# Performance work log

Measured on AMD Instinct MI355X. Metric: run time of the kernel, lower is better.

The kernel has to match this reference:

```python
import jax, jax.numpy as jnp
import numpy as np
from jax import lax

# ---- static config (matches init_kwargs) ----
STRIDE = 16
BASE_SIZE = 16
SCALES = np.array([2., 4., 8., 16., 32.])
RATIOS = np.array([0.5, 1., 2.])
CLIP = 4.14
NMS_THRESH = 0.7
PRE_NMS = 6000
POST_NMS = 300
MIN_SIZE = 16.0


def _whctrs(a):
    w = a[2] - a[0] + 1.0
    h = a[3] - a[1] + 1.0
    return w, h, a[0] + 0.5 * (w - 1.0), a[1] + 0.5 * (h - 1.0)


def _mkanchors(ws, hs, xc, yc):
    return np.stack([xc - 0.5 * (ws - 1.0), yc - 0.5 * (hs - 1.0),
                     xc + 0.5 * (ws - 1.0), yc + 0.5 * (hs - 1.0)], axis=1)


def _base_anchors():
    ba = np.array([1.0, 1.0, BASE_SIZE, BASE_SIZE]) - 1.0
    w, h, xc, yc = _whctrs(ba)
    size = w * h
    ws = np.round(np.sqrt(size / RATIOS))
    hs = np.round(ws * RATIOS)
    ra = _mkanchors(ws, hs, xc, yc)
    out = []
    for i in range(ra.shape[0]):
        w, h, xc, yc = _whctrs(ra[i])
        out.append(_mkanchors(w * SCALES, h * SCALES, xc, yc))
    return np.concatenate(out, axis=0)  # (A,4), A = len(ratios)*len(scales)


def _grid_anchors(Hf, Wf):
    ba = _base_anchors()                       # (A,4)
    sx, sy = np.meshgrid(np.arange(Wf) * STRIDE, np.arange(Hf) * STRIDE)
    shifts = np.stack([sx, sy, sx, sy], axis=-1)          # (Hf,Wf,4)
    anch = shifts[:, :, None, :] + ba[None, None, :, :]    # (Hf,Wf,A,4)
    return jnp.asarray(anch.reshape(1, -1, 4), dtype=jnp.float32)


def _decode_clip(anchors, deltas, img_h, img_w):
    # NormalizedBoxCenterDecoder (stds=1) + clip to image
    aw = anchors[..., 2] - anchors[..., 0]
    ah = anchors[..., 3] - anchors[..., 1]
    ax = anchors[..., 0] + 0.5 * aw
    ay = anchors[..., 1] + 0.5 * ah
    dx, dy, dw, dh = deltas[..., 0], deltas[..., 1], deltas[..., 2], deltas[..., 3]
    ox = dx * aw + ax
    oy = dy * ah + ay
    ow = jnp.exp(jnp.minimum(dw, CLIP)) * aw * 0.5
    oh = jnp.exp(jnp.minimum(dh, CLIP)) * ah * 0.5
    x1 = jnp.clip(ox - ow, 0.0, img_w - 1.0)
    y1 = jnp.clip(oy - oh, 0.0, img_h - 1.0)
    x2 = jnp.clip(ox + ow, 0.0, img_w - 1.0)
    y2 = jnp.clip(oy + oh, 0.0, img_h - 1.0)
    return jnp.stack([x1, y1, x2, y2], axis=-1)


def _nms_single(scores, boxes):
    # scores (N,), boxes (N,4). Greedy NMS, force_suppress, sorted by score desc.
    order = jnp.argsort(-scores)[:PRE_NMS]
    s = scores[order]
    b = boxes[order]
    x1, y1, x2, y2 = b[:, 0], b[:, 1], b[:, 2], b[:, 3]
    area = (x2 - x1) * (y2 - y1)
    iw = jnp.maximum(jnp.minimum(x2[:, None], x2[None, :]) - jnp.maximum(x1[:, None], x1[None, :]), 0.0)
    ih = jnp.maximum(jnp.minimum(y2[:, None], y2[None, :]) - jnp.maximum(y1[:, None], y1[None, :]), 0.0)
    inter = iw * ih
    iou = inter / (area[:, None] + area[None, :] - inter + 1e-12)  # (PRE,PRE)

    supp0 = s < 0.0  # invalid entries (score set to -1 by min_size filter)

    def body(supp, i):
        keep = jnp.logical_not(supp[i])
        new = jnp.where(keep, jnp.logical_or(supp, iou[i] > NMS_THRESH), supp)
        new = new.at[i].set(supp[i])  # never self-suppress
        return new, None

    supp, _ = lax.scan(body, supp0, jnp.arange(PRE_NMS))
    kept = jnp.logical_not(supp)
    perm = jnp.argsort(jnp.where(kept, 0, 1), stable=True)  # kept boxes first, order preserved
    out_s = jnp.where(kept[perm], s[perm], -1.0)
    out_b = jnp.where(kept[perm][:, None], b[perm], -1.0)
    return out_s[:POST_NMS, None], out_b[:POST_NMS]


def _forward(img, x, conv_w, conv_b, score_w, score_b, loc_w, loc_b):
    B, _, Hf, Wf = x.shape
    img_h, img_w = float(img.shape[2]), float(img.shape[3])
    anchors = _grid_anchors(Hf, Wf)  # (1, Hf*Wf*A, 4)

    # conv1 3x3 pad 1 + ReLU
    h = lax.conv_general_dilated(x, conv_w, (1, 1), [(1, 1), (1, 1)],
                                 dimension_numbers=('NCHW', 'OIHW', 'NCHW'))
    h = jax.nn.relu(h + conv_b[None, :, None, None])

    A = score_w.shape[0]
    raw_scores = jnp.einsum('bchw,oc->bhwo', h, score_w.reshape(A, -1)) + score_b
    raw_scores = raw_scores.reshape(B, -1, 1)                       # (B,N,1)
    raw_boxes = jnp.einsum('bchw,oc->bhwo', h, loc_w.reshape(4 * A, -1)) + loc_b
    raw_boxes = raw_boxes.reshape(B, -1, 4)                         # (B,N,4)

    rpn_scores = jax.nn.sigmoid(raw_scores)

    roi = _decode_clip(anchors, raw_boxes, img_h, img_w)            # (B,N,4)
    width = roi[..., 2] - roi[..., 0]
    height = roi[..., 3] - roi[..., 1]
    invalid = jnp.logical_or(width < MIN_SIZE, height < MIN_SIZE)   # (B,N)
    score = jnp.where(invalid[..., None], -1.0, rpn_scores)         # (B,N,1)
    roi = jnp.where(invalid[..., None], -1.0, roi)

    out_s, out_b = jax.vmap(_nms_single)(score[..., 0], roi)        # (B,300,1),(B,300,4)
    return jnp.concatenate([out_s, out_b], axis=-1)                 # (B,300,5)


def setup_inputs() -> dict:
    key = jax.random.key(0)
    ks = jax.random.split(key, 8)
    img = jax.random.normal(ks[0], (1, 3, 1024, 1024), jnp.float32)
    x = jax.random.normal(ks[1], (1, 1024, 64, 64), jnp.float32)
    conv_w = jax.random.normal(ks[2], (1024, 1024, 3, 3), jnp.float32) * 0.01
    conv_b = jnp.zeros((1024,), jnp.float32)
    score_w = jax.random.normal(ks[3], (15, 1024, 1, 1), jnp.float32) * 0.01
    score_b = jnp.zeros((15,), jnp.float32)
    loc_w = jax.random.normal(ks[4], (60, 1024, 1, 1), jnp.float32) * 0.002
    loc_b = jnp.zeros((60,), jnp.float32)
    return {"img": img, "x": x, "conv_w": conv_w, "conv_b": conv_b,
            "score_w": score_w, "score_b": score_b, "loc_w": loc_w, "loc_b": loc_b}


def reference(img, x, conv_w, conv_b, score_w, score_b, loc_w, loc_b):
    return _forward(img, x, conv_w, conv_b, score_w, score_b, loc_w, loc_b)
```

## Files before the change

kernel.cpp:

```cpp
#include <hip/hip_runtime.h>

typedef unsigned int uint;
typedef unsigned short ushort;
typedef unsigned long long u64;

typedef __attribute__((ext_vector_type(8))) short short8;
typedef __attribute__((ext_vector_type(4))) float floatx4;

__device__ inline ushort bf16rne(float v) {
  uint b = __float_as_uint(v);
  uint r = (b + 0x7fffu + ((b >> 16) & 1u)) >> 16;
  return (ushort)r;
}

__device__ inline void gl_lds16(const void* g, void* l) {
  __builtin_amdgcn_global_load_lds(
      (const __attribute__((address_space(1))) unsigned int*)g,
      (__attribute__((address_space(3))) unsigned int*)l, 16, 0, 0);
}

__global__ __launch_bounds__(256) void prep_x(const float* __restrict__ x,
                                              ushort* __restrict__ xh,
                                              ushort* __restrict__ xl) {
  __shared__ float tile[64 * 65];
  int ci0 = blockIdx.x * 64, y = blockIdx.y, t = threadIdx.x;
#pragma unroll
  for (int it = 0; it < 16; ++it) {
    int L = t + 256 * it;
    int cl = L >> 6, xx = L & 63;
    tile[cl * 65 + xx] = x[(size_t)(ci0 + cl) * 4096 + y * 64 + xx];
  }
  __syncthreads();
#pragma unroll
  for (int it = 0; it < 16; ++it) {
    int L = t + 256 * it;
    int xx = L >> 6, cl = L & 63;
    float v = tile[cl * 65 + xx];
    ushort h2 = bf16rne(v);
    float hf = __uint_as_float((uint)h2 << 16);
    ushort l2 = bf16rne(v - hf);
    size_t oi = ((size_t)((y + 1) * 66 + (xx + 1))) * 1024 + ci0 + cl;
    xh[oi] = h2;
    xl[oi] = l2;
  }
}

__global__ __launch_bounds__(256) void prep_w(const float* __restrict__ w,
                                              ushort* __restrict__ wh,
                                              ushort* __restrict__ wl) {
  __shared__ float tile[2304];
  int co = blockIdx.x, ci0 = blockIdx.y * 256, t = threadIdx.x;
  const float* src = w + ((size_t)co * 1024 + ci0) * 9;
  for (int i = t; i < 2304; i += 256) tile[i] = src[i];
  __syncthreads();
  int ci = ci0 + t;
#pragma unroll
  for (int off = 0; off < 9; ++off) {
    float v = tile[t * 9 + off];
    ushort h2 = bf16rne(v);
    float hf = __uint_as_float((uint)h2 << 16);
    ushort l2 = bf16rne(v - hf);
    size_t oi = ((size_t)off << 20) | ((size_t)co << 10) | (size_t)ci;
    wh[oi] = h2;
    wl[oi] = l2;
  }
}

__global__ __launch_bounds__(256) void prep_head(
    const float* __restrict__ score_w, const float* __restrict__ loc_w,
    const float* __restrict__ score_b, const float* __restrict__ loc_b,
    ushort* __restrict__ wh, ushort* __restrict__ wl, float* __restrict__ bh) {
  int idx = blockIdx.x * 256 + threadIdx.x;
  int o = idx >> 10, ci = idx & 1023;
  float v = 0.f;
  if (o < 15) v = score_w[o * 1024 + ci];
  else if (o < 75) v = loc_w[(o - 15) * 1024 + ci];
  ushort h2 = bf16rne(v);
  float hf = __uint_as_float((uint)h2 << 16);
  wh[idx] = h2;
  wl[idx] = bf16rne(v - hf);
  if (idx < 128) bh[idx] = (idx < 15) ? score_b[idx] : ((idx < 75) ? loc_b[idx - 15] : 0.f);
}

template <int IM2COL>
__global__ __launch_bounds__(256, 1) void gemm_bf16x3(
    const ushort* __restrict__ Ahi, const ushort* __restrict__ Alo,
    const ushort* __restrict__ Bhi, const ushort* __restrict__ Blo,
    const float* __restrict__ bias, int nChunks, float* __restrict__ outRaw,
    ushort* __restrict__ outHi, ushort* __restrict__ outLo) {
  __shared__ ushort sm[2 * 4 * 128 * 32];
  const int t = threadIdx.x;
  const int m0 = blockIdx.x * 128;
  const int n0 = blockIdx.y * 128;

  auto stage = [&](int kc, int bufIdx) {
    char* lds = (char*)sm + bufIdx * 32768;
    int off = 0, cc = 0, oy = 0, ox = 0;
    if (IM2COL) {
      off = kc >> 5;
      cc = (kc & 31) << 5;
      oy = off / 3;
      ox = off - 3 * oy;
    }
#pragma unroll
    for (int q = 0; q < 2; ++q) {
      int L = t + 256 * q, row = L >> 2, seg = L & 3;
      size_t aoff, boff;
      if (IM2COL) {
        int m = m0 + row, y = m >> 6, xq = m & 63;
        aoff = ((size_t)((y + oy) * 66 + (xq + ox)) * 1024 + (size_t)cc) * 2 + seg * 16;
        boff = (((size_t)off << 20) + ((size_t)(n0 + row) << 10) + (size_t)cc) * 2 + seg * 16;
      } else {
        aoff = (((size_t)(m0 + row) << 10) + (size_t)kc * 32) * 2 + seg * 16;
        boff = (((size_t)(n0 + row) << 10) + (size_t)kc * 32) * 2 + seg * 16;
      }
      int dst = L * 16;
      gl_lds16((const char*)Ahi + aoff, lds + dst);
      gl_lds16((const char*)Alo + aoff, lds + 8192 + dst);
      gl_lds16((const char*)Bhi + boff, lds + 16384 + dst);
      gl_lds16((const char*)Blo + boff, lds + 24576 + dst);
    }
  };

  const int lane = t & 63, wv = t >> 6;
  const int wm = (wv & 1) * 64, wn = (wv >> 1) * 64;
  const int arow = wm + (lane & 15);
  const int brow = wn + (lane & 15);
  const int ko = (lane >> 4) * 8;

  floatx4 acc[4][4];
#pragma unroll
  for (int i = 0; i < 4; ++i)
#pragma unroll
    for (int j = 0; j < 4; ++j) acc[i][j] = (floatx4){0.f, 0.f, 0.f, 0.f};

  stage(0, 0);
  for (int kc = 0; kc < nChunks; ++kc) {
    __syncthreads();
    if (kc + 1 < nChunks) stage(kc + 1, (kc + 1) & 1);
    const ushort* sb = sm + (kc & 1) * 16384;
    const ushort* sAh = sb;
    const ushort* sAl = sb + 4096;
    const ushort* sBh = sb + 8192;
    const ushort* sBl = sb + 12288;
    short8 ah[4], al[4], bh2[4], bl2[4];
#pragma unroll
    for (int i = 0; i < 4; ++i) {
      ah[i] = *(const short8*)(sAh + (arow + 16 * i) * 32 + ko);
      al[i] = *(const short8*)(sAl + (arow + 16 * i) * 32 + ko);
      bh2[i] = *(const short8*)(sBh + (brow + 16 * i) * 32 + ko);
      bl2[i] = *(const short8*)(sBl + (brow + 16 * i) * 32 + ko);
    }
#pragma unroll
    for (int i = 0; i < 4; ++i)
#pragma unroll
      for (int j = 0; j < 4; ++j) {
        acc[i][j] = __builtin_amdgcn_mfma_f32_16x16x32_bf16(ah[i], bh2[j], acc[i][j], 0, 0, 0);
        acc[i][j] = __builtin_amdgcn_mfma_f32_16x16x32_bf16(ah[i], bl2[j], acc[i][j], 0, 0, 0);
        acc[i][j] = __builtin_amdgcn_mfma_f32_16x16x32_bf16(al[i], bh2[j], acc[i][j], 0, 0, 0);
      }
  }

#pragma unroll
  for (int i = 0; i < 4; ++i)
#pragma unroll
    for (int j = 0; j < 4; ++j) {
      int nn = n0 + wn + 16 * j + (lane & 15);
      float bv = bias[nn];
#pragma unroll
      for (int r = 0; r < 4; ++r) {
        int mm = m0 + wm + 16 * i + (lane >> 4) * 4 + r;
        float v = acc[i][j][r] + bv;
        if (IM2COL) {
          v = fmaxf(v, 0.f);
          ushort h2 = bf16rne(v);
          float hf = __uint_as_float((uint)h2 << 16);
          ushort l2 = bf16rne(v - hf);
          outHi[(size_t)mm * 1024 + nn] = h2;
          outLo[(size_t)mm * 1024 + nn] = l2;
        } else {
          outRaw[(size_t)mm * 128 + nn] = v;
        }
      }
    }
}

__global__ __launch_bounds__(256) void decode_k(const float* __restrict__ raw,
                                                float* __restrict__ scores,
                                                float4* __restrict__ boxes,
                                                uint* __restrict__ key32,
                                                uint* __restrict__ hist) {
  int i = blockIdx.x * 256 + threadIdx.x;
  int m = i / 15, a = i - m * 15;
  int y = m >> 6, x = m & 63;
  const float* rp = raw + (size_t)m * 128;
  float logit = rp[a];
  float dx = rp[15 + 4 * a], dy = rp[16 + 4 * a];
  float dw = rp[17 + 4 * a], dh = rp[18 + 4 * a];
  int rr = a / 5, ss = a - rr * 5;
  float sc5 = (float)(2 << ss);
  float W = ((rr == 0) ? 23.f : (rr == 1) ? 16.f : 11.f) * sc5;
  float H = ((rr == 0) ? 12.f : (rr == 1) ? 16.f : 22.f) * sc5;
  float aw = W - 1.f, ah = H - 1.f;
  float ax = x * 16.f + 7.5f, ay = y * 16.f + 7.5f;
  float ox = dx * aw + ax, oyc = dy * ah + ay;
  float ow = expf(fminf(dw, 4.14f)) * aw * 0.5f;
  float oh = expf(fminf(dh, 4.14f)) * ah * 0.5f;
  float x1 = fminf(fmaxf(ox - ow, 0.f), 1023.f);
  float y1 = fminf(fmaxf(oyc - oh, 0.f), 1023.f);
  float x2 = fminf(fmaxf(ox + ow, 0.f), 1023.f);
  float y2 = fminf(fmaxf(oyc + oh, 0.f), 1023.f);
  bool inval = ((x2 - x1) < 16.f) || ((y2 - y1) < 16.f);
  float sc = inval ? -1.f : (1.f / (1.f + expf(-logit)));
  scores[i] = sc;
  boxes[i] = inval ? make_float4(-1.f, -1.f, -1.f, -1.f) : make_float4(x1, y1, x2, y2);
  uint kb = __float_as_uint(sc);
  uint key = (kb & 0x80000000u) ? ~kb : (kb | 0x80000000u);
  key32[i] = key;
  atomicAdd(&hist[key >> 16], 1u);
}

__global__ __launch_bounds__(256) void find_t16(const uint* __restrict__ hist,
                                                uint* __restrict__ selT) {
  __shared__ uint ps[256];
  __shared__ int segS;
  int t = threadIdx.x;
  uint s = 0;
  const uint* hp = hist + t * 256;
  for (int i = 0; i < 256; ++i) s += hp[i];
  ps[t] = s;
  __syncthreads();
  for (int d = 1; d < 256; d <<= 1) {
    uint v = ps[t] + ((t + d < 256) ? ps[t + d] : 0u);
    __syncthreads();
    ps[t] = v;
    __syncthreads();
  }
  if (ps[t] >= 6000u && (t == 255 || ps[t + 1] < 6000u)) segS = t;
  __syncthreads();
  int sg = segS;
  uint base = (sg == 255) ? 0u : ps[sg + 1];
  uint h2 = hist[sg * 256 + t];
  __syncthreads();
  ps[t] = h2;
  __syncthreads();
  for (int d = 1; d < 256; d <<= 1) {
    uint v = ps[t] + ((t + d < 256) ? ps[t + d] : 0u);
    __syncthreads();
    ps[t] = v;
    __syncthreads();
  }
  if (base + ps[t] >= 6000u && (t == 255 || base + ps[t + 1] < 6000u))
    *selT = (uint)(sg * 256 + t);
}

__global__ __launch_bounds__(256) void gather_k(const uint* __restrict__ key32,
                                                const uint* __restrict__ selT,
                                                uint* __restrict__ cnt,
                                                u64* __restrict__ cand) {
  int i = blockIdx.x * 256 + threadIdx.x;
  uint T = *selT;
  uint k = key32[i];
  if ((k >> 16) >= T) {
    uint pos = atomicAdd(cnt, 1u);
    if (pos < 8192) cand[pos] = ((u64)k << 32) | (u64)(~(uint)i);
  }
}

__global__ __launch_bounds__(1024) void sort_gather(
    const u64* __restrict__ cand, const uint* __restrict__ cnt,
    const float* __restrict__ scores, const float4* __restrict__ boxes,
    float* __restrict__ sortedS, float4* __restrict__ sortedB) {
  extern __shared__ u64 sk[];
  int t = threadIdx.x;
  int C = (int)*cnt;
  if (C > 8192) C = 8192;
  for (int j = t; j < 8192; j += 1024) sk[j] = (j < C) ? cand[j] : 0ull;
  __syncthreads();
  for (int k = 2; k <= 8192; k <<= 1) {
    for (int j2 = k >> 1; j2 > 0; j2 >>= 1) {
      for (int p = t; p < 4096; p += 1024) {
        int i = ((p & ~(j2 - 1)) << 1) | (p & (j2 - 1));
        int ix = i | j2;
        u64 a = sk[i], b = sk[ix];
        bool ddir = (i & k) != 0;
        if ((a < b) != ddir) { sk[i] = b; sk[ix] = a; }
      }
      __syncthreads();
    }
  }
  for (int j = t; j < 6016; j += 1024) {
    if (j < 6000) {
      u64 key = sk[j];
      uint idx = ~(uint)(key & 0xffffffffu);
      sortedS[j] = scores[idx];
      sortedB[j] = boxes[idx];
    } else {
      sortedS[j] = -1.f;
      sortedB[j] = make_float4(0.f, 0.f, 0.f, 0.f);
    }
  }
}

__global__ __launch_bounds__(64) void iou_mask(const float4* __restrict__ boxes,
                                               u64* __restrict__ mask) {
  __shared__ float cx1[64], cy1[64], cx2[64], cy2[64], car[64];
  int bi = blockIdx.x, bj = blockIdx.y, t = threadIdx.x;
  float4 cb = boxes[bj * 64 + t];
  cx1[t] = cb.x; cy1[t] = cb.y; cx2[t] = cb.z; cy2[t] = cb.w;
  car[t] = (cb.z - cb.x) * (cb.w - cb.y);
  __syncthreads();
  int r = bi * 64 + t;
  float4 rb = boxes[r];
  float ra = (rb.z - rb.x) * (rb.w - rb.y);
  u64 wd = 0;
#pragma unroll 8
  for (int j = 0; j < 64; ++j) {
    float iw = fmaxf(fminf(rb.z, cx2[j]) - fmaxf(rb.x, cx1[j]), 0.f);
    float ih = fmaxf(fminf(rb.w, cy2[j]) - fmaxf(rb.y, cy1[j]), 0.f);
    float inter = iw * ih;
    float iou = inter / (ra + car[j] - inter + 1e-12f);
    if (iou > 0.7f && r != bj * 64 + j) wd |= (1ull << j);
  }
  mask[(size_t)r * 128 + bj] = wd;
}

__global__ __launch_bounds__(64) void nms_scan(const u64* __restrict__ mask,
                                               const float* __restrict__ sortedS,
                                               const float4* __restrict__ sortedB,
                                               float* __restrict__ out) {
  __shared__ int klist[300];
  int lane = threadIdx.x;
  u64 Sx = 0, Sy = 0;
  for (int w2 = 0; w2 < 94; ++w2) {
    bool neg = sortedS[w2 * 64 + lane] < 0.f;
    u64 m2 = __ballot(neg);
    if ((w2 >> 1) == lane) { if (w2 & 1) Sy = m2; else Sx = m2; }
  }
  int count = 0;
  for (int w2 = 0; w2 < 94; ++w2) {
    u64 cur = __shfl((w2 & 1) ? Sy : Sx, w2 >> 1);
    u64 rem = ~cur;
    if (w2 == 93) rem &= (1ull << 48) - 1;
    while (rem) {
      int b = __builtin_ctzll(rem);
      int i = w2 * 64 + b;
      if (lane == 0) klist[count] = i;
      count++;
      if (count == 300) goto done;
      const ulonglong2* rp = (const ulonglong2*)(mask + (size_t)i * 128);
      ulonglong2 rv = rp[lane];
      Sx |= rv.x;
      Sy |= rv.y;
      u64 cur2 = __shfl((w2 & 1) ? Sy : Sx, w2 >> 1);
      rem &= ~cur2;
      rem &= (b == 63) ? 0ull : (~0ull << (b + 1));
    }
  }
done:
  __syncthreads();
  for (int j = lane; j < 300; j += 64) {
    float s;
    float4 bb;
    if (j < count) {
      int i = klist[j];
      s = sortedS[i];
      bb = sortedB[i];
    } else {
      s = -1.f;
      bb = make_float4(-1.f, -1.f, -1.f, -1.f);
    }
    out[j * 5 + 0] = s;
    out[j * 5 + 1] = bb.x;
    out[j * 5 + 2] = bb.y;
    out[j * 5 + 3] = bb.z;
    out[j * 5 + 4] = bb.w;
  }
}

constexpr size_t O_XH = 0;
constexpr size_t O_XL = 8921088;
constexpr size_t O_WTH = 17842176;
constexpr size_t O_WTL = 36716544;
constexpr size_t O_HH = 55590912;
constexpr size_t O_HL = 63979520;
constexpr size_t O_WHH = 72368128;
constexpr size_t O_WHL = 72630272;
constexpr size_t O_BHD = 72892416;
constexpr size_t O_SC = 72892928;
constexpr size_t O_BX = 73138688;
constexpr size_t O_KEY = 74121728;
constexpr size_t O_HIST = 74367488;
constexpr size_t O_CNT = 74629632;
constexpr size_t O_CAND = 74629888;
constexpr size_t O_SELT = 74695424;
constexpr size_t O_SS = 74695680;
constexpr size_t O_SB = 74719744;
constexpr size_t O_RAW = 0;
constexpr size_t O_MASK = 17842176;

extern "C" void kernel_launch(void* const* d_in, const int* in_sizes, int n_in,
                              void* d_out, int out_size, void* d_ws,
                              size_t ws_size, hipStream_t stream) {
  (void)in_sizes; (void)n_in; (void)out_size; (void)ws_size;
  const float* x = (const float*)d_in[1];
  const float* conv_w = (const float*)d_in[2];
  const float* conv_b = (const float*)d_in[3];
  const float* score_w = (const float*)d_in[4];
  const float* score_b = (const float*)d_in[5];
  const float* loc_w = (const float*)d_in[6];
  const float* loc_b = (const float*)d_in[7];
  float* out = (float*)d_out;
  char* ws = (char*)d_ws;

  ushort* xh = (ushort*)(ws + O_XH);
  ushort* xl = (ushort*)(ws + O_XL);
  ushort* wTh = (ushort*)(ws + O_WTH);
  ushort* wTl = (ushort*)(ws + O_WTL);
  ushort* hh = (ushort*)(ws + O_HH);
  ushort* hl = (ushort*)(ws + O_HL);
  ushort* wHh = (ushort*)(ws + O_WHH);
  ushort* wHl = (ushort*)(ws + O_WHL);
  float* biasH = (float*)(ws + O_BHD);
  float* raw = (float*)(ws + O_RAW);
  float* scores = (float*)(ws + O_SC);
  float4* boxes = (float4*)(ws + O_BX);
  uint* key32 = (uint*)(ws + O_KEY);
  uint* hist = (uint*)(ws + O_HIST);
  uint* cnt = (uint*)(ws + O_CNT);
  u64* cand = (u64*)(ws + O_CAND);
  uint* selT = (uint*)(ws + O_SELT);
  float* sortedS = (float*)(ws + O_SS);
  float4* sortedB = (float4*)(ws + O_SB);
  u64* mask = (u64*)(ws + O_MASK);

  hipMemsetAsync(ws + O_XH, 0, 2 * 8921088, stream);
  hipMemsetAsync(ws + O_HIST, 0, 262144 + 256, stream);

  prep_x<<<dim3(16, 64), 256, 0, stream>>>(x, xh, xl);
  prep_w<<<dim3(1024, 4), 256, 0, stream>>>(conv_w, wTh, wTl);
  prep_head<<<512, 256, 0, stream>>>(score_w, loc_w, score_b, loc_b, wHh, wHl, biasH);

  gemm_bf16x3<1><<<dim3(32, 8), 256, 0, stream>>>(xh, xl, wTh, wTl, conv_b, 288,
                                                  nullptr, hh, hl);
  gemm_bf16x3<0><<<dim3(32, 1), 256, 0, stream>>>(hh, hl, wHh, wHl, biasH, 32,
                                                  raw, nullptr, nullptr);

  decode_k<<<240, 256, 0, stream>>>(raw, scores, boxes, key32, hist);
  find_t16<<<1, 256, 0, stream>>>(hist, selT);
  gather_k<<<240, 256, 0, stream>>>(key32, selT, cnt, cand);
  sort_gather<<<1, 1024, 65536, stream>>>(cand, cnt, scores, boxes, sortedS, sortedB);
  iou_mask<<<dim3(94, 94), 64, 0, stream>>>(sortedB, mask);
  nms_scan<<<1, 64, 0, stream>>>(mask, sortedS, sortedB, out);
}
```

Before: 743.9 us.

## Swizzle GEMM LDS layout, replace bitonic sort with bucket rank, prune NMS work

The GEMM staging now writes LDS in MFMA-fragment order, so each lane reads a contiguous 16-byte slice and LDS bank conflicts drop. The single-block 8192-element bitonic sort is replaced by a 4096-bucket histogram scatter followed by an in-bucket rank, which cuts the many barrier-separated passes. The IoU mask kernel skips lower-triangle tiles that the scan never reads. The NMS scan prefetches the next candidate's mask row and stops early once 300 boxes are kept. The bucket rank costs quadratic work if many candidates share a bucket, and it uses an extra workspace buffer.

```diff
diff --git a/kernel.cpp b/kernel.cpp
--- a/kernel.cpp
+++ b/kernel.cpp
@@ -104,15 +104,17 @@
     }
 #pragma unroll
     for (int q = 0; q < 2; ++q) {
-      int L = t + 256 * q, row = L >> 2, seg = L & 3;
+      int L = t + 256 * q;
+      int g = L >> 6, ko = (L >> 4) & 3, row = L & 15;
+      int gr = g * 16 + row;
       size_t aoff, boff;
       if (IM2COL) {
-        int m = m0 + row, y = m >> 6, xq = m & 63;
-        aoff = ((size_t)((y + oy) * 66 + (xq + ox)) * 1024 + (size_t)cc) * 2 + seg * 16;
-        boff = (((size_t)off << 20) + ((size_t)(n0 + row) << 10) + (size_t)cc) * 2 + seg * 16;
+        int m = m0 + gr, y = m >> 6, xq = m & 63;
+        aoff = ((size_t)((y + oy) * 66 + (xq + ox)) * 1024 + (size_t)cc + ko * 8) * 2;
+        boff = (((size_t)off << 20) + ((size_t)(n0 + gr) << 10) + (size_t)cc + ko * 8) * 2;
       } else {
-        aoff = (((size_t)(m0 + row) << 10) + (size_t)kc * 32) * 2 + seg * 16;
-        boff = (((size_t)(n0 + row) << 10) + (size_t)kc * 32) * 2 + seg * 16;
+        aoff = (((size_t)(m0 + gr) << 10) + (size_t)kc * 32 + ko * 8) * 2;
+        boff = (((size_t)(n0 + gr) << 10) + (size_t)kc * 32 + ko * 8) * 2;
       }
       int dst = L * 16;
       gl_lds16((const char*)Ahi + aoff, lds + dst);
@@ -124,9 +126,6 @@
 
   const int lane = t & 63, wv = t >> 6;
   const int wm = (wv & 1) * 64, wn = (wv >> 1) * 64;
-  const int arow = wm + (lane & 15);
-  const int brow = wn + (lane & 15);
-  const int ko = (lane >> 4) * 8;
 
   floatx4 acc[4][4];
 #pragma unroll
@@ -146,10 +145,11 @@
     short8 ah[4], al[4], bh2[4], bl2[4];
 #pragma unroll
     for (int i = 0; i < 4; ++i) {
-      ah[i] = *(const short8*)(sAh + (arow + 16 * i) * 32 + ko);
-      al[i] = *(const short8*)(sAl + (arow + 16 * i) * 32 + ko);
-      bh2[i] = *(const short8*)(sBh + (brow + 16 * i) * 32 + ko);
-      bl2[i] = *(const short8*)(sBl + (brow + 16 * i) * 32 + ko);
+      int ga = (wm >> 4) + i, gb = (wn >> 4) + i;
+      ah[i] = *(const short8*)(sAh + ga * 512 + lane * 8);
+      al[i] = *(const short8*)(sAl + ga * 512 + lane * 8);
+      bh2[i] = *(const short8*)(sBh + gb * 512 + lane * 8);
+      bl2[i] = *(const short8*)(sBl + gb * 512 + lane * 8);
     }
 #pragma unroll
     for (int i = 0; i < 4; ++i)
@@ -267,45 +267,75 @@
   }
 }
 
-__global__ __launch_bounds__(1024) void sort_gather(
+__global__ __launch_bounds__(1024) void sort_rank(
     const u64* __restrict__ cand, const uint* __restrict__ cnt,
-    const float* __restrict__ scores, const float4* __restrict__ boxes,
+    const uint* __restrict__ selT, const float* __restrict__ scores,
+    const float4* __restrict__ boxes, u64* __restrict__ srt,
     float* __restrict__ sortedS, float4* __restrict__ sortedB) {
-  extern __shared__ u64 sk[];
+  __shared__ uint hist[4096];
+  __shared__ uint cbase[4096];
+  __shared__ uint cs[1024];
   int t = threadIdx.x;
-  int C = (int)*cnt;
-  if (C > 8192) C = 8192;
-  for (int j = t; j < 8192; j += 1024) sk[j] = (j < C) ? cand[j] : 0ull;
-  __syncthreads();
-  for (int k = 2; k <= 8192; k <<= 1) {
-    for (int j2 = k >> 1; j2 > 0; j2 >>= 1) {
-      for (int p = t; p < 4096; p += 1024) {
-        int i = ((p & ~(j2 - 1)) << 1) | (p & (j2 - 1));
-        int ix = i | j2;
-        u64 a = sk[i], b = sk[ix];
-        bool ddir = (i & k) != 0;
-        if ((a < b) != ddir) { sk[i] = b; sk[ix] = a; }
-      }
-      __syncthreads();
-    }
-  }
-  for (int j = t; j < 6016; j += 1024) {
-    if (j < 6000) {
-      u64 key = sk[j];
-      uint idx = ~(uint)(key & 0xffffffffu);
-      sortedS[j] = scores[idx];
-      sortedB[j] = boxes[idx];
-    } else {
-      sortedS[j] = -1.f;
-      sortedB[j] = make_float4(0.f, 0.f, 0.f, 0.f);
+  uint C = *cnt;
+  if (C > 8192u) C = 8192u;
+  uint b16 = (*selT) << 4;
+  for (int i = t; i < 4096; i += 1024) hist[i] = 0;
+  __syncthreads();
+  for (uint j = t; j < C; j += 1024) {
+    uint b = min((uint)(cand[j] >> 44) - b16, 4095u);
+    atomicAdd(&hist[b], 1u);
+  }
+  __syncthreads();
+  uint s = hist[4 * t] + hist[4 * t + 1] + hist[4 * t + 2] + hist[4 * t + 3];
+  cs[t] = s;
+  __syncthreads();
+  for (int d = 1; d < 1024; d <<= 1) {
+    uint v = cs[t] + ((t + d < 1024) ? cs[t + d] : 0u);
+    __syncthreads();
+    cs[t] = v;
+    __syncthreads();
+  }
+  uint above = (t < 1023) ? cs[t + 1] : 0u;
+  uint run = 0;
+  for (int i = 3; i >= 0; --i) {
+    cbase[4 * t + i] = above + run;
+    run += hist[4 * t + i];
+  }
+  __syncthreads();
+  for (int i = t; i < 4096; i += 1024) hist[i] = 0;
+  __syncthreads();
+  for (uint j = t; j < C; j += 1024) {
+    u64 e = cand[j];
+    uint b = min((uint)(e >> 44) - b16, 4095u);
+    uint pos = cbase[b] + atomicAdd(&hist[b], 1u);
+    srt[pos] = e;
+  }
+  __syncthreads();
+  if (t < 16) {
+    sortedS[6000 + t] = -1.f;
+    sortedB[6000 + t] = make_float4(0.f, 0.f, 0.f, 0.f);
+  }
+  for (uint j = t; j < C; j += 1024) {
+    u64 e = srt[j];
+    uint b = min((uint)(e >> 44) - b16, 4095u);
+    uint start = cbase[b], n = hist[b];
+    uint rank = 0;
+    for (uint q = 0; q < n; ++q) rank += (srt[start + q] > e) ? 1u : 0u;
+    uint pos = start + rank;
+    if (pos < 6000u) {
+      uint idx = ~(uint)(e & 0xffffffffu);
+      sortedS[pos] = scores[idx];
+      sortedB[pos] = boxes[idx];
     }
   }
 }
 
 __global__ __launch_bounds__(64) void iou_mask(const float4* __restrict__ boxes,
                                                u64* __restrict__ mask) {
+  int bi = blockIdx.x, bj = blockIdx.y;
+  if (bj < bi) return;
   __shared__ float cx1[64], cy1[64], cx2[64], cy2[64], car[64];
-  int bi = blockIdx.x, bj = blockIdx.y, t = threadIdx.x;
+  int t = threadIdx.x;
   float4 cb = boxes[bj * 64 + t];
   cx1[t] = cb.x; cy1[t] = cb.y; cx2[t] = cb.z; cy2[t] = cb.w;
   car[t] = (cb.z - cb.x) * (cb.w - cb.y);
@@ -329,7 +359,7 @@
                                                const float* __restrict__ sortedS,
                                                const float4* __restrict__ sortedB,
                                                float* __restrict__ out) {
-  __shared__ int klist[300];
+  __shared__ int klist[304];
   int lane = threadIdx.x;
   u64 Sx = 0, Sy = 0;
   for (int w2 = 0; w2 < 94; ++w2) {
@@ -338,26 +368,35 @@
     if ((w2 >> 1) == lane) { if (w2 & 1) Sy = m2; else Sx = m2; }
   }
   int count = 0;
-  for (int w2 = 0; w2 < 94; ++w2) {
+  for (int w2 = 0; w2 < 94 && count < 300; ++w2) {
     u64 cur = __shfl((w2 & 1) ? Sy : Sx, w2 >> 1);
     u64 rem = ~cur;
     if (w2 == 93) rem &= (1ull << 48) - 1;
+    int pf_i = -1;
+    ulonglong2 pf;
     while (rem) {
       int b = __builtin_ctzll(rem);
       int i = w2 * 64 + b;
+      u64 rem2 = (b == 63) ? 0ull : (rem & (~0ull << (b + 1)));
+      ulonglong2 rv;
+      if (i == pf_i) rv = pf;
+      else rv = ((const ulonglong2*)(mask + (size_t)i * 128))[lane];
+      if (rem2) {
+        int nb = __builtin_ctzll(rem2);
+        pf_i = w2 * 64 + nb;
+        pf = ((const ulonglong2*)(mask + (size_t)pf_i * 128))[lane];
+      } else {
+        pf_i = -1;
+      }
       if (lane == 0) klist[count] = i;
       count++;
-      if (count == 300) goto done;
-      const ulonglong2* rp = (const ulonglong2*)(mask + (size_t)i * 128);
-      ulonglong2 rv = rp[lane];
+      if (count == 300) break;
       Sx |= rv.x;
       Sy |= rv.y;
       u64 cur2 = __shfl((w2 & 1) ? Sy : Sx, w2 >> 1);
-      rem &= ~cur2;
-      rem &= (b == 63) ? 0ull : (~0ull << (b + 1));
-    }
-  }
-done:
+      rem = rem2 & ~cur2;
+    }
+  }
   __syncthreads();
   for (int j = lane; j < 300; j += 64) {
     float s;
@@ -398,6 +437,7 @@
 constexpr size_t O_SB = 74719744;
 constexpr size_t O_RAW = 0;
 constexpr size_t O_MASK = 17842176;
+constexpr size_t O_SRT = 24002560;
 
 extern "C" void kernel_launch(void* const* d_in, const int* in_sizes, int n_in,
                               void* d_out, int out_size, void* d_ws,
@@ -432,6 +472,7 @@
   uint* selT = (uint*)(ws + O_SELT);
   float* sortedS = (float*)(ws + O_SS);
   float4* sortedB = (float4*)(ws + O_SB);
+  u64* srt = (u64*)(ws + O_SRT);
   u64* mask = (u64*)(ws + O_MASK);
 
   hipMemsetAsync(ws + O_XH, 0, 2 * 8921088, stream);
@@ -449,7 +490,8 @@
   decode_k<<<240, 256, 0, stream>>>(raw, scores, boxes, key32, hist);
   find_t16<<<1, 256, 0, stream>>>(hist, selT);
   gather_k<<<240, 256, 0, stream>>>(key32, selT, cnt, cand);
-  sort_gather<<<1, 1024, 65536, stream>>>(cand, cnt, scores, boxes, sortedS, sortedB);
+  sort_rank<<<1, 1024, 0, stream>>>(cand, cnt, selT, scores, boxes, srt,
+                                    sortedS, sortedB);
   iou_mask<<<dim3(94, 94), 64, 0, stream>>>(sortedB, mask);
   nms_scan<<<1, 64, 0, stream>>>(mask, sortedS, sortedB, out);
 }
```

New measurement: 823.5 us. 1.11x slower.
